# Optimization experiments

Measured on AMD Instinct MI355X. Metric: run time of the kernel, lower is better.

Reference implementation:

```python
import jax, jax.numpy as jnp
import numpy as np

HEADS = 8
DIM_HEAD = 64
DIM = 512
SCALE = DIM ** -0.5  # NOTE: original scales by dim**-0.5, not dim_head**-0.5


def setup_inputs() -> dict:
    key = jax.random.key(0)
    k1, k2, k3 = jax.random.split(key, 3)
    b, n = 2, 4096
    x = jax.random.normal(k1, (b, n, DIM), dtype=jnp.float32)
    Wqkv = jax.random.normal(k2, (DIM, 3 * HEADS * DIM_HEAD), dtype=jnp.float32) * (DIM ** -0.5)
    Wout = jax.random.normal(k3, (HEADS * DIM_HEAD, DIM), dtype=jnp.float32) * ((HEADS * DIM_HEAD) ** -0.5)
    b_out = jnp.zeros((DIM,), dtype=jnp.float32)
    return {"x": x, "Wqkv": Wqkv, "Wout": Wout, "b_out": b_out}


def reference(x, Wqkv, Wout, b_out):
    b, n, _ = x.shape
    h, d = HEADS, DIM_HEAD
    qkv = x @ Wqkv  # [b, n, 3*h*d]
    q, k, v = jnp.split(qkv, 3, axis=-1)
    to_heads = lambda t: t.reshape(b, n, h, d).transpose(0, 2, 1, 3)  # [b,h,n,d]
    q, k, v = to_heads(q), to_heads(k), to_heads(v)
    half = n // 2
    q_s, q_t = q[:, :, :half], q[:, :, half:]
    k_t = k[:, :, half:]  # k_s is unused in the original module
    v_s, v_t = v[:, :, :half], v[:, :, half:]
    # temporal branch: q_t attends to k_t, reads v_t
    dots_t = jnp.einsum('bhid,bhjd->bhij', q_t, k_t) * SCALE
    # spatial branch: cross-term q_s attends to k_t, reads v_s
    dots_s = jnp.einsum('bhid,bhjd->bhij', q_s, k_t) * SCALE
    attn_s = jax.nn.softmax(dots_s, axis=-1)
    attn_t = jax.nn.softmax(dots_t, axis=-1)
    out_s = jnp.einsum('bhij,bhjd->bhid', attn_s, v_s)
    out_t = jnp.einsum('bhij,bhjd->bhid', attn_t, v_t)
    out = jnp.concatenate([out_s, out_t], axis=2)  # [b,h,n,d]
    out = out.transpose(0, 2, 1, 3).reshape(b, n, h * d)
    return out @ Wout + b_out
```

## Files before the change

### kernel.cpp

```cpp
#include <hip/hip_runtime.h>
#include <hip/hip_bf16.h>

typedef __bf16 bf16;
typedef _Float16 f16;
typedef __bf16 bf16x4 __attribute__((ext_vector_type(4)));
typedef __bf16 bf16x8 __attribute__((ext_vector_type(8)));
typedef _Float16 f16x4 __attribute__((ext_vector_type(4)));
typedef _Float16 f16x8 __attribute__((ext_vector_type(8)));
typedef float floatx4 __attribute__((ext_vector_type(4)));

static __device__ __forceinline__ floatx4 mfma_bf16(bf16x8 a, bf16x8 b, floatx4 c) {
  return __builtin_amdgcn_mfma_f32_16x16x32_bf16(a, b, c, 0, 0, 0);
}
static __device__ __forceinline__ floatx4 mfma_f16k32(f16x8 a, f16x8 b, floatx4 c) {
  return __builtin_amdgcn_mfma_f32_16x16x32_f16(a, b, c, 0, 0, 0);
}

static __device__ __forceinline__ void async16(void* lds, const void* gp) {
  __builtin_amdgcn_global_load_lds(
      (const __attribute__((address_space(1))) void*)gp,
      (__attribute__((address_space(3))) void*)lds, 16, 0, 0);
}

static __device__ __forceinline__ bf16x8 cvt8(float4 f0, float4 f1) {
  bf16x8 r;
  r[0] = (bf16)f0.x; r[1] = (bf16)f0.y; r[2] = (bf16)f0.z; r[3] = (bf16)f0.w;
  r[4] = (bf16)f1.x; r[5] = (bf16)f1.y; r[6] = (bf16)f1.z; r[7] = (bf16)f1.w;
  return r;
}

#define HEADS 8
#define DIMH 64
#define DIM 512
#define SEQ 4096
#define HALF 2048
#define BATCH 2
#define MROWS (BATCH * SEQ)
#define ELEMS ((size_t)MROWS * DIM)
#define NPARTS 4

#define C2F (0.044194173824159216f * 1.4426950408889634f)

__global__ __launch_bounds__(256)
void prep(const float* __restrict__ X, bf16* __restrict__ Xb,
          const float* __restrict__ wqkv, bf16* __restrict__ W1t,
          const float* __restrict__ wout, bf16* __restrict__ W2t) {
  __shared__ float tile[32][33];
  const int bid = blockIdx.x, t = threadIdx.x;
  if (bid < 2048) {
    size_t i = ((size_t)bid * 256 + t) * 8;
    float4 f0 = *reinterpret_cast<const float4*>(X + i);
    float4 f1 = *reinterpret_cast<const float4*>(X + i + 4);
    *reinterpret_cast<bf16x8*>(Xb + i) = cvt8(f0, f1);
    return;
  }
  const float* src; bf16* dst; int N, id;
  if (bid < 2816) { id = bid - 2048; src = wqkv; dst = W1t; N = 1536; }
  else            { id = bid - 2816; src = wout; dst = W2t; N = 512; }
  const int nb = N / 32;
  const int n0 = (id % nb) * 32, k0 = (id / nb) * 32;
  const int r = t >> 3, c4 = (t & 7) * 4;
  float4 v = *reinterpret_cast<const float4*>(src + (size_t)(k0 + r) * N + n0 + c4);
  tile[r][c4 + 0] = v.x; tile[r][c4 + 1] = v.y;
  tile[r][c4 + 2] = v.z; tile[r][c4 + 3] = v.w;
  __syncthreads();
  bf16x4 o;
#pragma unroll
  for (int i = 0; i < 4; ++i) o[i] = (bf16)tile[c4 + i][r];
  *reinterpret_cast<bf16x4*>(dst + (size_t)(n0 + r) * DIM + k0 + c4) = o;
}

__global__ __launch_bounds__(256)
void qkv_gemm(const bf16* __restrict__ Xb, const bf16* __restrict__ Wt,
              bf16* __restrict__ Qw, bf16* __restrict__ Kw, f16* __restrict__ Vt) {
  __shared__ __align__(16) char smem_raw[36864];

  const int m0 = blockIdx.x * 128, n0 = blockIdx.y * 128;
  const int t = threadIdx.x;
  const int wave = t >> 6, lane = t & 63, quad = lane >> 4, l16 = lane & 15;
  const int wr = wave >> 1, wc = wave & 1;

  f16 (*Ts)[72] = (f16(*)[72])(smem_raw + wave * 9216);

  floatx4 acc[4][4] = {};

  auto issue = [&](int buf, int k0) {
    bf16* Asf = (bf16*)(smem_raw + buf * 16384);
    bf16* Bsf = Asf + 4096;
#pragma unroll
    for (int it = 0; it < 2; ++it) {
      int g = it * 256 + t, row = g >> 2, c8 = (g & 3) * 8;
      async16(Asf + (size_t)g * 8, Xb + (size_t)(m0 + row) * DIM + k0 + c8);
      async16(Bsf + (size_t)g * 8, Wt + (size_t)(n0 + row) * DIM + k0 + c8);
    }
  };

  issue(0, 0);
  int buf = 0;
#pragma unroll 1
  for (int k0 = 0; k0 < DIM; k0 += 32) {
    __syncthreads();
    if (k0 + 32 < DIM) issue(buf ^ 1, k0 + 32);

    const bf16* Asf = (const bf16*)(smem_raw + buf * 16384);
    const bf16* Bsf = Asf + 4096;
    bf16x8 af[4], bfr[4];
#pragma unroll
    for (int mi = 0; mi < 4; ++mi)
      af[mi] = *reinterpret_cast<const bf16x8*>(
          Asf + (size_t)(wr * 64 + mi * 16 + l16) * 32 + quad * 8);
#pragma unroll
    for (int ni = 0; ni < 4; ++ni)
      bfr[ni] = *reinterpret_cast<const bf16x8*>(
          Bsf + (size_t)(wc * 64 + ni * 16 + l16) * 32 + quad * 8);
#pragma unroll
    for (int mi = 0; mi < 4; ++mi)
#pragma unroll
      for (int ni = 0; ni < 4; ++ni)
        acc[mi][ni] = mfma_bf16(af[mi], bfr[ni], acc[mi][ni]);
    buf ^= 1;
  }

  if (n0 < 1024) {
#pragma unroll
    for (int mi = 0; mi < 4; ++mi)
#pragma unroll
      for (int ni = 0; ni < 4; ++ni)
#pragma unroll
        for (int r = 0; r < 4; ++r) {
          int row = m0 + wr * 64 + mi * 16 + quad * 4 + r;
          int col = n0 + wc * 64 + ni * 16 + l16;
          int which = col >> 9, cc = col & 511;
          int head = cc >> 6, dim = cc & 63;
          int bb = row >> 12, nn = row & 4095;
          float val = acc[mi][ni][r];
          if (which == 0) val *= C2F;
          bf16* dst = which ? Kw : Qw;
          dst[(((size_t)(bb * HEADS + head)) * SEQ + nn) * DIMH + dim] = (bf16)val;
        }
  } else {
    __syncthreads();
    int head = (n0 + wc * 64 - 1024) >> 6;
#pragma unroll
    for (int mi = 0; mi < 4; ++mi)
#pragma unroll
      for (int ni = 0; ni < 4; ++ni) {
        f16x4 pv;
#pragma unroll
        for (int r = 0; r < 4; ++r) pv[r] = (f16)acc[mi][ni][r];
        *reinterpret_cast<f16x4*>(&Ts[ni * 16 + l16][mi * 16 + quad * 4]) = pv;
      }
    int bb = m0 >> 12, nnb = (m0 + wr * 64) & 4095;
    size_t base = ((size_t)(bb * HEADS + head)) * DIMH;
#pragma unroll
    for (int it = 0; it < 8; ++it) {
      int idx = lane + it * 64;
      int d = idx >> 3, ns = (idx & 7) * 8;
      *reinterpret_cast<f16x8*>(Vt + (base + d) * SEQ + nnb + ns) =
          *reinterpret_cast<const f16x8*>(&Ts[d][ns]);
    }
  }
}

__global__ __launch_bounds__(256)
void attn_kernel(const bf16* __restrict__ Q, const bf16* __restrict__ K,
                 const f16* __restrict__ Vt, f16* __restrict__ Opart,
                 float* __restrict__ Lpart) {
  const int qt = blockIdx.x;
  const int h = blockIdx.y;
  const int bb = blockIdx.z >> 2, part = blockIdx.z & 3;
  const int t = threadIdx.x;
  const int wave = t >> 6, lane = t & 63, quad = lane >> 4, l16 = lane & 15;

  __shared__ bf16 Ks[64][72];
  __shared__ f16 VsT[64][72];

  const size_t hb = ((size_t)(bb * HEADS + h)) * SEQ * DIMH;
  const int vhalf = (qt < 16) ? 0 : HALF;
  const int kstart = HALF + part * 512;
  const int vstart = vhalf + part * 512;
  const int q0 = qt * 128 + wave * 32;

  bf16x8 qa[2][2];
#pragma unroll
  for (int mt = 0; mt < 2; ++mt)
#pragma unroll
    for (int kc = 0; kc < 2; ++kc)
      qa[mt][kc] = *reinterpret_cast<const bf16x8*>(
          Q + hb + (size_t)(q0 + mt * 16 + l16) * DIMH + kc * 32 + quad * 8);

  floatx4 o_acc[2][4] = {};
  float l_acc[2] = {0.f, 0.f};

  int srow[2], sdst[2], g8s;
  {
    int r0 = t >> 3;  g8s = (t & 7) * 8;
#pragma unroll
    for (int it = 0; it < 2; ++it) {
      int row = r0 + it * 32;
      int g32 = row >> 5, w = row & 31, q = w >> 3, j = w & 7;
      int m = (j < 4) ? (4 * q + j) : (16 + 4 * q + (j - 4));
      srow[it] = row;
      sdst[it] = 32 * g32 + m;
    }
  }

  bf16x8 kreg[2];
  f16x8 vreg[2];
  auto loadc = [&](int kc0) {
#pragma unroll
    for (int it = 0; it < 2; ++it) {
      kreg[it] = *reinterpret_cast<const bf16x8*>(
          K + hb + (size_t)(kstart + kc0 + srow[it]) * DIMH + g8s);
      vreg[it] = *reinterpret_cast<const f16x8*>(
          Vt + hb + (size_t)srow[it] * SEQ + vstart + kc0 + g8s);
    }
  };

  loadc(0);
#pragma unroll 1
  for (int kc0 = 0; kc0 < 512; kc0 += 64) {
    __syncthreads();
#pragma unroll
    for (int it = 0; it < 2; ++it) {
      *reinterpret_cast<bf16x8*>(&Ks[sdst[it]][g8s]) = kreg[it];
      *reinterpret_cast<f16x8*>(&VsT[srow[it]][g8s]) = vreg[it];
    }
    __syncthreads();
    int nxt = kc0 + 64; if (nxt >= 512) nxt = 0;
    loadc(nxt);

#pragma unroll
    for (int g = 0; g < 2; ++g) {
      bf16x8 kaA0 = *reinterpret_cast<const bf16x8*>(&Ks[g * 32 + l16][quad * 8]);
      bf16x8 kaA1 = *reinterpret_cast<const bf16x8*>(&Ks[g * 32 + l16][32 + quad * 8]);
      bf16x8 kaB0 = *reinterpret_cast<const bf16x8*>(&Ks[g * 32 + 16 + l16][quad * 8]);
      bf16x8 kaB1 = *reinterpret_cast<const bf16x8*>(&Ks[g * 32 + 16 + l16][32 + quad * 8]);

      f16x8 pbm[2];
#pragma unroll
      for (int mt = 0; mt < 2; ++mt) {
        floatx4 stA = {0.f, 0.f, 0.f, 0.f}, stB = {0.f, 0.f, 0.f, 0.f};
        stA = mfma_bf16(kaA0, qa[mt][0], stA);
        stA = mfma_bf16(kaA1, qa[mt][1], stA);
        stB = mfma_bf16(kaB0, qa[mt][0], stB);
        stB = mfma_bf16(kaB1, qa[mt][1], stB);
        float ls = l_acc[mt];
        f16x8 pb;
#pragma unroll
        for (int r = 0; r < 4; ++r) {
          float pA = __builtin_amdgcn_exp2f(stA[r]);
          float pB = __builtin_amdgcn_exp2f(stB[r]);
          ls += pA + pB;
          pb[r] = (f16)pA;
          pb[4 + r] = (f16)pB;
        }
        l_acc[mt] = ls;
        pbm[mt] = pb;
      }

#pragma unroll
      for (int dsub = 0; dsub < 4; ++dsub) {
        f16x8 va = *reinterpret_cast<const f16x8*>(
            &VsT[dsub * 16 + l16][g * 32 + quad * 8]);
        o_acc[0][dsub] = mfma_f16k32(va, pbm[0], o_acc[0][dsub]);
        o_acc[1][dsub] = mfma_f16k32(va, pbm[1], o_acc[1][dsub]);
      }
    }
  }

  f16* Op = Opart + (size_t)part * ELEMS;
  float* Lp = Lpart + (size_t)part * MROWS * HEADS;
#pragma unroll
  for (int mt = 0; mt < 2; ++mt) {
    float v = l_acc[mt];
    v += __shfl_xor(v, 16);
    v += __shfl_xor(v, 32);
    int n = q0 + mt * 16 + l16;
    size_t rowidx = (size_t)(bb * SEQ + n);
    if (quad == 0) Lp[rowidx * HEADS + h] = v;
    size_t rowbase = rowidx * DIM + h * DIMH;
#pragma unroll
    for (int dsub = 0; dsub < 4; ++dsub) {
      f16x4 ov;
#pragma unroll
      for (int r = 0; r < 4; ++r) ov[r] = (f16)o_acc[mt][dsub][r];
      *reinterpret_cast<f16x4*>(Op + rowbase + dsub * 16 + quad * 4) = ov;
    }
  }
}

__global__ __launch_bounds__(256)
void out_gemm(const f16* __restrict__ Opart, const float* __restrict__ Lpart,
              const bf16* __restrict__ Wt, const float* __restrict__ bias,
              float* __restrict__ out) {
  __shared__ __align__(16) bf16 Asf[64 * 64];
  __shared__ __align__(16) bf16 Bsf[64 * 64];

  const int m0 = blockIdx.x * 64, n0 = blockIdx.y * 64;
  const int t = threadIdx.x;
  const int wave = t >> 6, lane = t & 63, quad = lane >> 4, l16 = lane & 15;
  const int m_off = (wave >> 1) * 32, n_off = (wave & 1) * 32;

  int srowi[2], sc8[2];
#pragma unroll
  for (int it = 0; it < 2; ++it) {
    int g = t + it * 256;
    srowi[it] = g >> 3; sc8[it] = (g & 7) * 8;
  }

  float linv[2][8];
#pragma unroll
  for (int it = 0; it < 2; ++it) {
    size_t ar = (size_t)(m0 + srowi[it]);
#pragma unroll
    for (int hh = 0; hh < 8; ++hh) {
      float s = 0.f;
#pragma unroll
      for (int p = 0; p < NPARTS; ++p)
        s += Lpart[(size_t)p * MROWS * HEADS + ar * HEADS + hh];
      linv[it][hh] = 1.0f / s;
    }
  }

  floatx4 acc[2][2] = {};

  f16x8 oreg[2][NPARTS];
  auto loadO = [&](int k0) {
#pragma unroll
    for (int it = 0; it < 2; ++it) {
      size_t abase = (size_t)(m0 + srowi[it]) * DIM + k0 + sc8[it];
#pragma unroll
      for (int p = 0; p < NPARTS; ++p)
        oreg[it][p] = *reinterpret_cast<const f16x8*>(Opart + (size_t)p * ELEMS + abase);
    }
  };

  loadO(0);
#pragma unroll 1
  for (int k0 = 0; k0 < DIM; k0 += 64) {
#pragma unroll
    for (int it = 0; it < 2; ++it) {
      int g = t + it * 256;
      async16(Bsf + (size_t)g * 8, Wt + (size_t)(n0 + srowi[it]) * DIM + k0 + sc8[it]);
      float inv = linv[it][(k0 + sc8[it]) >> 6];
      bf16x8 a;
#pragma unroll
      for (int j = 0; j < 8; ++j)
        a[j] = (bf16)(((float)oreg[it][0][j] + (float)oreg[it][1][j] +
                       (float)oreg[it][2][j] + (float)oreg[it][3][j]) * inv);
      *reinterpret_cast<bf16x8*>(Asf + (size_t)g * 8) = a;
    }
    __syncthreads();
    int nk = k0 + 64; if (nk >= DIM) nk = 0;
    loadO(nk);

#pragma unroll
    for (int kk = 0; kk < 2; ++kk) {
      bf16x8 a0 = *reinterpret_cast<const bf16x8*>(Asf + (size_t)(m_off + l16) * 64 + kk * 32 + quad * 8);
      bf16x8 a1 = *reinterpret_cast<const bf16x8*>(Asf + (size_t)(m_off + 16 + l16) * 64 + kk * 32 + quad * 8);
      bf16x8 b0 = *reinterpret_cast<const bf16x8*>(Bsf + (size_t)(n_off + l16) * 64 + kk * 32 + quad * 8);
      bf16x8 b1 = *reinterpret_cast<const bf16x8*>(Bsf + (size_t)(n_off + 16 + l16) * 64 + kk * 32 + quad * 8);
      acc[0][0] = mfma_bf16(a0, b0, acc[0][0]);
      acc[0][1] = mfma_bf16(a0, b1, acc[0][1]);
      acc[1][0] = mfma_bf16(a1, b0, acc[1][0]);
      acc[1][1] = mfma_bf16(a1, b1, acc[1][1]);
    }
    __syncthreads();
  }

#pragma unroll
  for (int mi = 0; mi < 2; ++mi)
#pragma unroll
    for (int ni = 0; ni < 2; ++ni)
#pragma unroll
      for (int r = 0; r < 4; ++r) {
        int row = m0 + m_off + mi * 16 + quad * 4 + r;
        int col = n0 + n_off + ni * 16 + l16;
        out[(size_t)row * DIM + col] = acc[mi][ni][r] + bias[col];
      }
}

extern "C" void kernel_launch(void* const* d_in, const int* in_sizes, int n_in,
                              void* d_out, int out_size, void* d_ws, size_t ws_size,
                              hipStream_t stream) {
  const float* x = (const float*)d_in[0];
  const float* wqkv = (const float*)d_in[1];
  const float* wout = (const float*)d_in[2];
  const float* bout = (const float*)d_in[3];
  float* out = (float*)d_out;

  char* ws = (char*)d_ws;
  f16* Opart = (f16*)ws;
  bf16* Xb = (bf16*)ws;
  bf16* Qw = (bf16*)(ws + ((size_t)32 << 20));
  bf16* Kw = Qw + ELEMS;
  f16* Vt = (f16*)(Kw + ELEMS);
  bf16* WtQKV = (bf16*)(Vt + ELEMS);
  bf16* WtOUT = WtQKV + (size_t)1536 * 512;
  float* Lpart = (float*)(WtOUT + (size_t)512 * 512);

  prep<<<3072, 256, 0, stream>>>(x, Xb, wqkv, WtQKV, wout, WtOUT);
  qkv_gemm<<<dim3(MROWS / 128, 1536 / 128), 256, 0, stream>>>(Xb, WtQKV, Qw, Kw, Vt);
  attn_kernel<<<dim3(SEQ / 128, HEADS, BATCH * NPARTS), 256, 0, stream>>>(Qw, Kw, Vt, Opart, Lpart);
  out_gemm<<<dim3(MROWS / 64, DIM / 64), 256, 0, stream>>>(Opart, Lpart, WtOUT, bout, out);
}
```

Baseline: 161.4 us.

## Stream K/V tiles into LDS with async global_load_lds double buffering

```diff
diff --git a/kernel.cpp b/kernel.cpp
--- a/kernel.cpp
+++ b/kernel.cpp
@@ -5,6 +5,7 @@
 typedef _Float16 f16;
 typedef __bf16 bf16x4 __attribute__((ext_vector_type(4)));
 typedef __bf16 bf16x8 __attribute__((ext_vector_type(8)));
+typedef _Float16 f16x2 __attribute__((ext_vector_type(2)));
 typedef _Float16 f16x4 __attribute__((ext_vector_type(4)));
 typedef _Float16 f16x8 __attribute__((ext_vector_type(8)));
 typedef float floatx4 __attribute__((ext_vector_type(4)));
@@ -166,15 +167,14 @@
 void attn_kernel(const bf16* __restrict__ Q, const bf16* __restrict__ K,
                  const f16* __restrict__ Vt, f16* __restrict__ Opart,
                  float* __restrict__ Lpart) {
+  __shared__ __align__(16) char smem[16384];
+
   const int qt = blockIdx.x;
   const int h = blockIdx.y;
   const int bb = blockIdx.z >> 2, part = blockIdx.z & 3;
   const int t = threadIdx.x;
   const int wave = t >> 6, lane = t & 63, quad = lane >> 4, l16 = lane & 15;
 
-  __shared__ bf16 Ks[64][72];
-  __shared__ f16 VsT[64][72];
-
   const size_t hb = ((size_t)(bb * HEADS + h)) * SEQ * DIMH;
   const int vhalf = (qt < 16) ? 0 : HALF;
   const int kstart = HALF + part * 512;
@@ -192,81 +192,74 @@
   floatx4 o_acc[2][4] = {};
   float l_acc[2] = {0.f, 0.f};
 
-  int srow[2], sdst[2], g8s;
-  {
-    int r0 = t >> 3;  g8s = (t & 7) * 8;
-#pragma unroll
-    for (int it = 0; it < 2; ++it) {
-      int row = r0 + it * 32;
-      int g32 = row >> 5, w = row & 31, q = w >> 3, j = w & 7;
-      int m = (j < 4) ? (4 * q + j) : (16 + 4 * q + (j - 4));
-      srow[it] = row;
-      sdst[it] = 32 * g32 + m;
-    }
-  }
-
-  bf16x8 kreg[2];
-  f16x8 vreg[2];
-  auto loadc = [&](int kc0) {
-#pragma unroll
-    for (int it = 0; it < 2; ++it) {
-      kreg[it] = *reinterpret_cast<const bf16x8*>(
-          K + hb + (size_t)(kstart + kc0 + srow[it]) * DIMH + g8s);
-      vreg[it] = *reinterpret_cast<const f16x8*>(
-          Vt + hb + (size_t)srow[it] * SEQ + vstart + kc0 + g8s);
-    }
+  const int r = t >> 3;
+  const int rr = r & 15;
+  const int kappa = (rr >> 2) * 8 + (rr & 3) + ((r & 16) ? 4 : 0);
+  const int kchunk = (t & 7) ^ (r & 7);
+  const bf16* kSrc = K + hb + (size_t)(kstart + kappa) * DIMH + kchunk * 8;
+
+  const int vd = t >> 2;
+  const int vchunk = (t & 3) ^ ((vd >> 1) & 3);
+  const f16* vSrc = Vt + hb + (size_t)vd * SEQ + vstart + vchunk * 8;
+
+  char* ldsK = smem + t * 16;
+  char* ldsV = smem + 4096 + t * 16;
+
+  auto issue = [&](int buf, int kc0) {
+    async16(ldsK + buf * 8192, kSrc + (size_t)kc0 * DIMH);
+    async16(ldsV + buf * 8192, vSrc + kc0);
   };
 
-  loadc(0);
+  const int koffA = l16 * 128 + ((quad ^ (l16 & 7)) * 16);
+  const int voff = l16 * 64 + ((quad ^ ((l16 >> 1) & 3)) * 16);
+
+  auto compute = [&](const char* Kb) {
+    const char* Vb = Kb + 4096;
+    bf16x8 kaA0 = *reinterpret_cast<const bf16x8*>(Kb + koffA);
+    bf16x8 kaA1 = *reinterpret_cast<const bf16x8*>(Kb + (koffA ^ 64));
+    bf16x8 kaB0 = *reinterpret_cast<const bf16x8*>(Kb + 2048 + koffA);
+    bf16x8 kaB1 = *reinterpret_cast<const bf16x8*>(Kb + 2048 + (koffA ^ 64));
+
+    f16x8 pbm[2];
+#pragma unroll
+    for (int mt = 0; mt < 2; ++mt) {
+      floatx4 stA = {0.f, 0.f, 0.f, 0.f}, stB = {0.f, 0.f, 0.f, 0.f};
+      stA = mfma_bf16(kaA0, qa[mt][0], stA);
+      stA = mfma_bf16(kaA1, qa[mt][1], stA);
+      stB = mfma_bf16(kaB0, qa[mt][0], stB);
+      stB = mfma_bf16(kaB1, qa[mt][1], stB);
+      float ls = l_acc[mt];
+      f16x8 pb;
+#pragma unroll
+      for (int rr2 = 0; rr2 < 4; ++rr2) {
+        float pA = __builtin_amdgcn_exp2f(stA[rr2]);
+        float pB = __builtin_amdgcn_exp2f(stB[rr2]);
+        ls += pA + pB;
+        pb[rr2] = (f16)pA;
+        pb[4 + rr2] = (f16)pB;
+      }
+      l_acc[mt] = ls;
+      pbm[mt] = pb;
+    }
+#pragma unroll
+    for (int dsub = 0; dsub < 4; ++dsub) {
+      f16x8 va = *reinterpret_cast<const f16x8*>(Vb + voff + dsub * 1024);
+      o_acc[0][dsub] = mfma_f16k32(va, pbm[0], o_acc[0][dsub]);
+      o_acc[1][dsub] = mfma_f16k32(va, pbm[1], o_acc[1][dsub]);
+    }
+  };
+
+  issue(0, 0);
 #pragma unroll 1
   for (int kc0 = 0; kc0 < 512; kc0 += 64) {
-    __syncthreads();
-#pragma unroll
-    for (int it = 0; it < 2; ++it) {
-      *reinterpret_cast<bf16x8*>(&Ks[sdst[it]][g8s]) = kreg[it];
-      *reinterpret_cast<f16x8*>(&VsT[srow[it]][g8s]) = vreg[it];
-    }
-    __syncthreads();
-    int nxt = kc0 + 64; if (nxt >= 512) nxt = 0;
-    loadc(nxt);
-
-#pragma unroll
-    for (int g = 0; g < 2; ++g) {
-      bf16x8 kaA0 = *reinterpret_cast<const bf16x8*>(&Ks[g * 32 + l16][quad * 8]);
-      bf16x8 kaA1 = *reinterpret_cast<const bf16x8*>(&Ks[g * 32 + l16][32 + quad * 8]);
-      bf16x8 kaB0 = *reinterpret_cast<const bf16x8*>(&Ks[g * 32 + 16 + l16][quad * 8]);
-      bf16x8 kaB1 = *reinterpret_cast<const bf16x8*>(&Ks[g * 32 + 16 + l16][32 + quad * 8]);
-
-      f16x8 pbm[2];
-#pragma unroll
-      for (int mt = 0; mt < 2; ++mt) {
-        floatx4 stA = {0.f, 0.f, 0.f, 0.f}, stB = {0.f, 0.f, 0.f, 0.f};
-        stA = mfma_bf16(kaA0, qa[mt][0], stA);
-        stA = mfma_bf16(kaA1, qa[mt][1], stA);
-        stB = mfma_bf16(kaB0, qa[mt][0], stB);
-        stB = mfma_bf16(kaB1, qa[mt][1], stB);
-        float ls = l_acc[mt];
-        f16x8 pb;
-#pragma unroll
-        for (int r = 0; r < 4; ++r) {
-          float pA = __builtin_amdgcn_exp2f(stA[r]);
-          float pB = __builtin_amdgcn_exp2f(stB[r]);
-          ls += pA + pB;
-          pb[r] = (f16)pA;
-          pb[4 + r] = (f16)pB;
-        }
-        l_acc[mt] = ls;
-        pbm[mt] = pb;
-      }
-
-#pragma unroll
-      for (int dsub = 0; dsub < 4; ++dsub) {
-        f16x8 va = *reinterpret_cast<const f16x8*>(
-            &VsT[dsub * 16 + l16][g * 32 + quad * 8]);
-        o_acc[0][dsub] = mfma_f16k32(va, pbm[0], o_acc[0][dsub]);
-        o_acc[1][dsub] = mfma_f16k32(va, pbm[1], o_acc[1][dsub]);
-      }
-    }
+    asm volatile("s_waitcnt vmcnt(0)" ::: "memory");
+    __syncthreads();
+    issue(1, kc0 + 32);
+    compute(smem);
+    asm volatile("s_waitcnt vmcnt(0)" ::: "memory");
+    __syncthreads();
+    if (kc0 + 64 < 512) issue(0, kc0 + 64);
+    compute(smem + 8192);
   }
 
   f16* Op = Opart + (size_t)part * ELEMS;
@@ -284,7 +277,7 @@
     for (int dsub = 0; dsub < 4; ++dsub) {
       f16x4 ov;
 #pragma unroll
-      for (int r = 0; r < 4; ++r) ov[r] = (f16)o_acc[mt][dsub][r];
+      for (int r2 = 0; r2 < 4; ++r2) ov[r2] = (f16)o_acc[mt][dsub][r2];
       *reinterpret_cast<f16x4*>(Op + rowbase + dsub * 16 + quad * 4) = ov;
     }
   }
```

After: 159.7 us. No clear change (-1.0%).
